# Kernel optimization log

Measured on AMD Instinct MI355X. Metric: run time of the kernel, lower is better.

The kernel has to match this reference:

```python
import jax, jax.numpy as jnp
import numpy as np

GAMMA = 0.5      # temperature from __init__
SOS_ID = 2       # constant <sos> token id
EPS = 1e-10


def setup_inputs() -> dict:
    key = jax.random.key(0)
    ks = jax.random.split(key, 12)
    B, T, E, DY, DZ, V = 64, 32, 100, 200, 500, 32000
    H = DY + DZ
    s = lambda k, shape, sc=1.0: (jax.random.normal(k, shape, jnp.float32) * sc)
    return {
        "z": s(ks[0], (B, DZ), 0.1),
        "labels": jax.random.uniform(ks[1], (B,), jnp.float32),
        "W_fc": s(ks[2], (DY, 1), 0.1),
        "b_fc": s(ks[3], (DY,), 0.1),
        "embed_weight": s(ks[4], (V, E), 0.1),
        "W_ih": s(ks[5], (3 * H, E), 0.05),
        "W_hh": s(ks[6], (3 * H, H), 0.05),
        "b_ih": s(ks[7], (3 * H,), 0.05),
        "b_hh": s(ks[8], (3 * H,), 0.05),
        "W_out": s(ks[9], (V, H), 0.05),
        "b_out": s(ks[10], (V,), 0.05),
        "gumbel_u": jax.random.uniform(ks[11], (T - 1, B, V), jnp.float32),
        "src": jax.random.randint(jax.random.fold_in(key, 99), (T, B), 0, V),
        "src_len": T,
    }


def _gru_step(h, x, W_ih, W_hh, b_ih, b_hh):
    # PyTorch GRU cell: gates ordered (r, z, n)
    gi = x @ W_ih.T + b_ih          # [B, 3H]
    gh = h @ W_hh.T + b_hh          # [B, 3H]
    i_r, i_z, i_n = jnp.split(gi, 3, axis=-1)
    h_r, h_z, h_n = jnp.split(gh, 3, axis=-1)
    r = jax.nn.sigmoid(i_r + h_r)
    zt = jax.nn.sigmoid(i_z + h_z)
    n = jnp.tanh(i_n + r * h_n)
    return (1.0 - zt) * n + zt * h


def reference(z, labels, W_fc, b_fc, embed_weight, W_ih, W_hh, b_ih, b_hh,
              W_out, b_out, gumbel_u, src, src_len):
    B, H = z.shape[0], W_hh.shape[1]
    V = W_out.shape[0]
    # h0 = cat(fc(1 - labels), z)
    h0 = jnp.concatenate([(1.0 - labels)[:, None] @ W_fc.T + b_fc, z], axis=-1)  # [B, H]
    x0 = jnp.broadcast_to(embed_weight[SOS_ID], (B, embed_weight.shape[1]))      # [B, E]

    def step(carry, u):
        h, x = carry
        h = _gru_step(h, x, W_ih, W_hh, b_ih, b_hh)      # [B, H]
        pred = h @ W_out.T + b_out                        # [B, V]
        g = -jnp.log(-jnp.log(u + EPS) + EPS)             # gumbel noise
        y = jax.nn.softmax(pred + g, axis=-1)             # gumbel_softmax, tau=1
        x_next = (y / GAMMA) @ embed_weight               # soft embedding [B, E]
        return (h, x_next), (h, pred)

    (_, _), (outs, preds) = jax.lax.scan(step, (h0, x0), gumbel_u)  # [T-1,B,H], [T-1,B,V]

    dt = z.dtype
    outputs = jnp.concatenate(
        [h0[None], jnp.zeros((1, B, H), dt), outs], axis=0)         # [T+1, B, H]
    predictions = jnp.concatenate(
        [jnp.zeros((1, B, V), dt), preds], axis=0)                  # [T, B, V]
    return outputs, predictions
```

## Files before the change

kernel.cpp:

```cpp
#include <hip/hip_runtime.h>

#define B 64
#define TS 31
#define E 100
#define DY 200
#define DZ 500
#define V 32000
#define H 700
#define HP 704
#define H3 2100
#define XH 800
#define SOS 2
#define OUT_PRED_OFF (33*B*H)
#define NPB 500
#define VCH 125
#define NVCH 256
#define SOFF 15.0f

typedef unsigned short u16;
typedef __attribute__((ext_vector_type(8))) short short8;
typedef __attribute__((ext_vector_type(4))) float f32x4;

__device__ __forceinline__ float sigm(float x) { return 1.f / (1.f + __expf(-x)); }
__device__ __forceinline__ u16 f2b(float f) {
  union { float f; unsigned int u; } c; c.f = f;
  unsigned int u = c.u;
  u16 h = (u16)(u >> 16);
  unsigned int rem = u & 0xFFFFu;
  h += (u16)((rem > 0x8000u) || (rem == 0x8000u && (h & 1)));
  return h;
}

__global__ __launch_bounds__(256) void k_zero(float* __restrict__ out, long n) {
  long i0 = (long)blockIdx.x * 256 + threadIdx.x;
  long st = (long)gridDim.x * 256;
  for (long i = i0; i < n; i += st) out[i] = 0.f;
}

__global__ __launch_bounds__(256) void k0_init(
    const float* __restrict__ z, const float* __restrict__ labels,
    const float* __restrict__ W_fc, const float* __restrict__ b_fc,
    const float* __restrict__ embed, const float* __restrict__ W_ih,
    const float* __restrict__ W_hh, const float* __restrict__ W_out,
    float* __restrict__ out, float* __restrict__ hA, float* __restrict__ WT,
    u16* __restrict__ W2, u16* __restrict__ h_bf,
    float* __restrict__ xacc, float* __restrict__ Zp, float* __restrict__ gh)
{
  long i0 = (long)blockIdx.x * 256 + threadIdx.x;
  long st = (long)gridDim.x * 256;
  for (long i = i0; i < (long)NPB * B; i += st) Zp[i] = 2.f / (float)NPB;
  for (long i = i0; i < (long)B * H3; i += st) gh[i] = 0.f;
  for (long i = i0; i < (long)B * V; i += st) out[OUT_PRED_OFF + i] = 0.f;
  for (long i = i0; i < (long)B * H; i += st) out[B * H + i] = 0.f;
  for (long i = i0; i < (long)B * H; i += st) {
    int b = (int)(i / H), j = (int)(i % H);
    float v = (j < DY) ? (1.f - labels[b]) * W_fc[j] + b_fc[j]
                       : z[b * DZ + (j - DY)];
    hA[i] = v;
    out[i] = v;
  }
  for (long i = i0; i < (long)B * E; i += st) {
    int e = (int)(i % E);
    xacc[i] = embed[SOS * E + e];
  }
  for (long i = i0; i < (long)B * HP; i += st) h_bf[i] = 0;
  for (long i = i0; i < (long)XH * H3; i += st) {
    int k = (int)(i / H3), g = (int)(i % H3);
    WT[i] = (k < E) ? W_ih[(long)g * E + k] : W_hh[(long)g * H + (k - E)];
  }
  for (long i = i0; i < (long)V * HP; i += st) {
    long s8 = i >> 3; int j = (int)(i & 7);
    int lane = (int)(s8 & 63);
    long tmp = s8 >> 6;
    int kk = (int)(tmp % 22);
    long cgrp = tmp / 22;
    int col = (int)(cgrp * 16 + (lane & 15));
    int k = kk * 32 + ((lane >> 4) << 3) + j;
    W2[i] = (k < H) ? f2b(W_out[(size_t)col * H + k]) : (u16)0;
  }
}

__global__ __launch_bounds__(256) void k1a(
    const float* __restrict__ xacc, const float* __restrict__ Zp,
    const float* __restrict__ hin, const float* __restrict__ WT,
    const float* __restrict__ b_ih,
    float* __restrict__ gig, float* __restrict__ gh)
{
  int nt = blockIdx.x, c = blockIdx.y;
  int n = nt * 32 + (threadIdx.x & 31);
  int bq = threadIdx.x >> 5;
  __shared__ float xs[64][100];
  __shared__ float invZ[64];
  if (c == 0) {
    if (threadIdx.x < 64) {
      float s = 0.f;
      for (int u = 0; u < NPB; ++u) s += Zp[(size_t)u * 64 + threadIdx.x];
      invZ[threadIdx.x] = 2.f / s;
    }
    __syncthreads();
  }
  for (int i = threadIdx.x; i < 6400; i += 256) {
    int b = i / 100, kk = i % 100;
    xs[b][kk] = (c == 0) ? xacc[i] * invZ[b] : hin[b * H + (c - 1) * 100 + kk];
  }
  __syncthreads();
  if (n >= H3) return;
  float acc[8];
  #pragma unroll
  for (int bb = 0; bb < 8; ++bb) acc[bb] = 0.f;
  for (int kk = 0; kk < 100; ++kk) {
    float w = WT[(size_t)(c * 100 + kk) * H3 + n];
    #pragma unroll
    for (int bb = 0; bb < 8; ++bb) acc[bb] += xs[bq * 8 + bb][kk] * w;
  }
  if (c == 0) {
    float bi = b_ih[n];
    #pragma unroll
    for (int bb = 0; bb < 8; ++bb) gig[(size_t)(bq * 8 + bb) * H3 + n] = acc[bb] + bi;
  } else {
    #pragma unroll
    for (int bb = 0; bb < 8; ++bb)
      atomicAdd(&gh[(size_t)(bq * 8 + bb) * H3 + n], acc[bb]);
  }
}

__global__ __launch_bounds__(256) void k1br(
    const float* __restrict__ gig, float* __restrict__ gh,
    const float* __restrict__ b_hh, const float* __restrict__ hin,
    float* __restrict__ hout, float* __restrict__ out_h, u16* __restrict__ h_bf,
    float* __restrict__ xacc)
{
  int i = blockIdx.x * 256 + threadIdx.x;
  if (i >= B * H) return;
  if (i < B * E) xacc[i] = 0.f;
  int b = i / H, j = i % H;
  size_t g0 = (size_t)b * H3 + j;
  float ir = gig[g0], iz = gig[g0 + H], in_ = gig[g0 + 2 * H];
  float hr = gh[g0] + b_hh[j];
  float hz = gh[g0 + H] + b_hh[H + j];
  float hn = gh[g0 + 2 * H] + b_hh[2 * H + j];
  gh[g0] = 0.f; gh[g0 + H] = 0.f; gh[g0 + 2 * H] = 0.f;
  float hprev = hin[b * H + j];
  float r  = sigm(ir + hr);
  float zt = sigm(iz + hz);
  float nn = tanhf(in_ + r * hn);
  float hv = (1.f - zt) * nn + zt * hprev;
  hout[b * H + j] = hv;
  out_h[i] = hv;
  h_bf[b * HP + j] = f2b(hv);
}

__global__ __launch_bounds__(256) void k2(
    const u16* __restrict__ h_bf, const u16* __restrict__ W2,
    const float* __restrict__ b_out, const float* __restrict__ gu,
    float* __restrict__ pred, float* __restrict__ w_f, float* __restrict__ Zp)
{
  __shared__ float lzp[64][4];
  const int u = blockIdx.x, tid = threadIdx.x;
  const int wave = tid >> 6, lane = tid & 63, l15 = lane & 15;
  const int col = u * 64 + wave * 16 + l15;
  f32x4 acc[4];
  #pragma unroll
  for (int q = 0; q < 4; ++q) acc[q] = f32x4{0.f, 0.f, 0.f, 0.f};
  const short8* wv2 = (const short8*)W2 + ((size_t)(u * 4 + wave) * 22) * 64 + lane;
  const u16* hp = h_bf + ((lane >> 4) << 3);
  for (int kk = 0; kk < 22; ++kk) {
    short8 bv = wv2[(size_t)kk * 64];
    #pragma unroll
    for (int rt = 0; rt < 4; ++rt) {
      short8 a = *reinterpret_cast<const short8*>(hp + (size_t)(rt * 16 + l15) * HP + kk * 32);
      acc[rt] = __builtin_amdgcn_mfma_f32_16x16x32_bf16(a, bv, acc[rt], 0, 0, 0);
    }
  }
  float bo = b_out[col];
  #pragma unroll
  for (int rt = 0; rt < 4; ++rt) {
    #pragma unroll
    for (int r = 0; r < 4; ++r) {
      int brow = rt * 16 + ((lane >> 4) << 2) + r;
      float pv = acc[rt][r] + bo;
      size_t off = (size_t)brow * V + col;
      __builtin_nontemporal_store(pv, &pred[off]);
      float uu = __builtin_nontemporal_load(&gu[off]);
      float g = -__logf(-__logf(uu + 1e-10f) + 1e-10f);
      float w = __expf(pv + g - SOFF);
      w_f[off] = w;
      float vz = w;
      vz += __shfl_xor(vz, 1); vz += __shfl_xor(vz, 2);
      vz += __shfl_xor(vz, 4); vz += __shfl_xor(vz, 8);
      if (l15 == 0) lzp[brow][wave] = vz;
    }
  }
  __syncthreads();
  if (tid < 64)
    Zp[(size_t)u * 64 + tid] = lzp[tid][0] + lzp[tid][1] + lzp[tid][2] + lzp[tid][3];
}

__global__ __launch_bounds__(256) void k3(
    const float* __restrict__ w_f, const float* __restrict__ embed,
    float* __restrict__ xacc)
{
  int c = blockIdx.x;
  int v0 = c * VCH;
  int e = threadIdx.x & 127, bh = threadIdx.x >> 7;
  __shared__ float ys[64][VCH];
  for (int i = threadIdx.x; i < 64 * VCH; i += 256) {
    int b = i / VCH, vv = i % VCH;
    ys[b][vv] = w_f[(size_t)b * V + v0 + vv];
  }
  __syncthreads();
  if (e >= E) return;
  float acc[32];
  #pragma unroll
  for (int bb = 0; bb < 32; ++bb) acc[bb] = 0.f;
  for (int vv = 0; vv < VCH; ++vv) {
    float w = embed[(size_t)(v0 + vv) * E + e];
    #pragma unroll
    for (int bb = 0; bb < 32; ++bb) acc[bb] += ys[bh * 32 + bb][vv] * w;
  }
  #pragma unroll
  for (int bb = 0; bb < 32; ++bb)
    atomicAdd(&xacc[(size_t)(bh * 32 + bb) * E + e], acc[bb]);
}

extern "C" void kernel_launch(void* const* d_in, const int* in_sizes, int n_in,
                              void* d_out, int out_size, void* d_ws, size_t ws_size,
                              hipStream_t stream) {
  (void)ws_size;
  float* out = (float*)d_out;

  static const long lsz[12] = {32000, 64, 200, 200, 3200000, 210000, 1470000,
                               2100, 2100, 22400000, 32000, 63488000};
  static const int dictP[12]    = {0, 1, 2, 3, 4, 5, 6, 7, 8, 9, 10, 11};
  static const int alpha14P[12] = {13, 10, 0, 4, 8, 2, 1, 6, 5, 3, 7, 9};
  static const int alpha12P[12] = {11, 10, 0, 4, 8, 2, 1, 6, 5, 3, 7, 9};
  auto okperm = [&](const int* p) -> bool {
    for (int i = 0; i < 12; ++i) {
      if (p[i] >= n_in) return false;
      if ((long)in_sizes[p[i]] != lsz[i]) return false;
    }
    return true;
  };
  const int* P_ = nullptr;
  if (okperm(dictP)) P_ = dictP;
  else if (okperm(alpha14P)) P_ = alpha14P;
  else if (okperm(alpha12P)) P_ = alpha12P;
  if (!P_) { k_zero<<<2048, 256, 0, stream>>>(out, (long)out_size); return; }

  const float* z      = (const float*)d_in[P_[0]];
  const float* labels = (const float*)d_in[P_[1]];
  const float* W_fc   = (const float*)d_in[P_[2]];
  const float* b_fc   = (const float*)d_in[P_[3]];
  const float* embed  = (const float*)d_in[P_[4]];
  const float* W_ih   = (const float*)d_in[P_[5]];
  const float* W_hh   = (const float*)d_in[P_[6]];
  const float* b_ih   = (const float*)d_in[P_[7]];
  const float* b_hh   = (const float*)d_in[P_[8]];
  const float* W_out  = (const float*)d_in[P_[9]];
  const float* b_out  = (const float*)d_in[P_[10]];
  const float* gu     = (const float*)d_in[P_[11]];

  char* w = (char*)d_ws;
  auto alloc = [&](size_t bytes) { char* p = w; w += (bytes + 255) & ~(size_t)255; return p; };
  float* hA    = (float*)alloc((size_t)B * H * 4);
  float* hB    = (float*)alloc((size_t)B * H * 4);
  float* WT    = (float*)alloc((size_t)XH * H3 * 4);
  float* gig   = (float*)alloc((size_t)B * H3 * 4);
  float* gh    = (float*)alloc((size_t)B * H3 * 4);
  float* w_f   = (float*)alloc((size_t)B * V * 4);
  float* Zp    = (float*)alloc((size_t)NPB * B * 4);
  float* xacc  = (float*)alloc((size_t)B * E * 4);
  u16*  W2     = (u16*)alloc((size_t)V * HP * 2);
  u16*  h_bf   = (u16*)alloc((size_t)B * HP * 2);

  k0_init<<<2048, 256, 0, stream>>>(z, labels, W_fc, b_fc, embed, W_ih, W_hh, W_out,
                                    out, hA, WT, W2, h_bf, xacc, Zp, gh);

  for (int t = 0; t < TS; ++t) {
    float* hin  = (t & 1) ? hB : hA;
    float* hout = (t & 1) ? hA : hB;
    float* pred = out + OUT_PRED_OFF + (size_t)(1 + t) * B * V;
    k1a<<<dim3(66, 8), 256, 0, stream>>>(xacc, Zp, hin, WT, b_ih, gig, gh);
    k1br<<<(B * H + 255) / 256, 256, 0, stream>>>(gig, gh, b_hh, hin, hout,
                                                  out + (size_t)(2 + t) * B * H, h_bf,
                                                  xacc);
    k2<<<NPB, 256, 0, stream>>>(h_bf, W2, b_out, gu + (size_t)t * B * V,
                                pred, w_f, Zp);
    if (t < TS - 1)
      k3<<<NVCH, 256, 0, stream>>>(w_f, embed, xacc);
  }
}
```

Measured before the change: 3.656 ms.

## Halve k2 block size to 1000 blocks and move softmax-denominator reduction into k3

The vocab-projection kernel now runs 1000 blocks of two waves each instead of 500 blocks of four, so the 32000-column GEMM spreads across more workgroups on the CUs. The per-batch partition-sum reduction, which used to be a serial 500-element loop in k1a's first block, now runs in the otherwise idle threads of k3. Those threads write four partial sums per batch row, and k1a just adds them. This takes a serial reduction off the critical path at the cost of more partial sums and extra work in k3's spare lanes.

New measurement: 5.249 ms. 43.6% more time.

```diff
diff --git a/kernel.cpp b/kernel.cpp
--- a/kernel.cpp
+++ b/kernel.cpp
@@ -12,7 +12,7 @@
 #define XH 800
 #define SOS 2
 #define OUT_PRED_OFF (33*B*H)
-#define NPB 500
+#define NPB2 1000
 #define VCH 125
 #define NVCH 256
 #define SOFF 15.0f
@@ -44,11 +44,11 @@
     const float* __restrict__ W_hh, const float* __restrict__ W_out,
     float* __restrict__ out, float* __restrict__ hA, float* __restrict__ WT,
     u16* __restrict__ W2, u16* __restrict__ h_bf,
-    float* __restrict__ xacc, float* __restrict__ Zp, float* __restrict__ gh)
+    float* __restrict__ xacc, float* __restrict__ ZpH, float* __restrict__ gh)
 {
   long i0 = (long)blockIdx.x * 256 + threadIdx.x;
   long st = (long)gridDim.x * 256;
-  for (long i = i0; i < (long)NPB * B; i += st) Zp[i] = 2.f / (float)NPB;
+  for (long i = i0; i < 4 * B; i += st) ZpH[i] = 0.5f;
   for (long i = i0; i < (long)B * H3; i += st) gh[i] = 0.f;
   for (long i = i0; i < (long)B * V; i += st) out[OUT_PRED_OFF + i] = 0.f;
   for (long i = i0; i < (long)B * H; i += st) out[B * H + i] = 0.f;
@@ -81,7 +81,7 @@
 }
 
 __global__ __launch_bounds__(256) void k1a(
-    const float* __restrict__ xacc, const float* __restrict__ Zp,
+    const float* __restrict__ xacc, const float* __restrict__ ZpH,
     const float* __restrict__ hin, const float* __restrict__ WT,
     const float* __restrict__ b_ih,
     float* __restrict__ gig, float* __restrict__ gh)
@@ -93,9 +93,8 @@
   __shared__ float invZ[64];
   if (c == 0) {
     if (threadIdx.x < 64) {
-      float s = 0.f;
-      for (int u = 0; u < NPB; ++u) s += Zp[(size_t)u * 64 + threadIdx.x];
-      invZ[threadIdx.x] = 2.f / s;
+      const float* zp = ZpH + threadIdx.x * 4;
+      invZ[threadIdx.x] = 2.f / (zp[0] + zp[1] + zp[2] + zp[3]);
     }
     __syncthreads();
   }
@@ -150,19 +149,20 @@
   h_bf[b * HP + j] = f2b(hv);
 }
 
-__global__ __launch_bounds__(256) void k2(
+__global__ __launch_bounds__(128) void k2(
     const u16* __restrict__ h_bf, const u16* __restrict__ W2,
     const float* __restrict__ b_out, const float* __restrict__ gu,
     float* __restrict__ pred, float* __restrict__ w_f, float* __restrict__ Zp)
 {
-  __shared__ float lzp[64][4];
+  __shared__ float lzp[64][2];
   const int u = blockIdx.x, tid = threadIdx.x;
   const int wave = tid >> 6, lane = tid & 63, l15 = lane & 15;
-  const int col = u * 64 + wave * 16 + l15;
+  const int cgrp = u * 2 + wave;
+  const int col = cgrp * 16 + l15;
   f32x4 acc[4];
   #pragma unroll
   for (int q = 0; q < 4; ++q) acc[q] = f32x4{0.f, 0.f, 0.f, 0.f};
-  const short8* wv2 = (const short8*)W2 + ((size_t)(u * 4 + wave) * 22) * 64 + lane;
+  const short8* wv2 = (const short8*)W2 + ((size_t)cgrp * 22) * 64 + lane;
   const u16* hp = h_bf + ((lane >> 4) << 3);
   for (int kk = 0; kk < 22; ++kk) {
     short8 bv = wv2[(size_t)kk * 64];
@@ -193,12 +193,13 @@
   }
   __syncthreads();
   if (tid < 64)
-    Zp[(size_t)u * 64 + tid] = lzp[tid][0] + lzp[tid][1] + lzp[tid][2] + lzp[tid][3];
+    Zp[(size_t)u * 64 + tid] = lzp[tid][0] + lzp[tid][1];
 }
 
 __global__ __launch_bounds__(256) void k3(
     const float* __restrict__ w_f, const float* __restrict__ embed,
-    float* __restrict__ xacc)
+    float* __restrict__ xacc, const float* __restrict__ Zp,
+    float* __restrict__ ZpH)
 {
   int c = blockIdx.x;
   int v0 = c * VCH;
@@ -209,7 +210,16 @@
     ys[b][vv] = w_f[(size_t)b * V + v0 + vv];
   }
   __syncthreads();
-  if (e >= E) return;
+  if (e >= E) {
+    if (e < 102 && c < 64) {
+      int id2 = (e - 100) * 2 + bh;
+      float s = 0.f;
+      for (int u = id2 * 250; u < id2 * 250 + 250; ++u)
+        s += Zp[(size_t)u * 64 + c];
+      ZpH[c * 4 + id2] = s;
+    }
+    return;
+  }
   float acc[32];
   #pragma unroll
   for (int bb = 0; bb < 32; ++bb) acc[bb] = 0.f;
@@ -268,25 +278,26 @@
   float* gig   = (float*)alloc((size_t)B * H3 * 4);
   float* gh    = (float*)alloc((size_t)B * H3 * 4);
   float* w_f   = (float*)alloc((size_t)B * V * 4);
-  float* Zp    = (float*)alloc((size_t)NPB * B * 4);
+  float* Zp    = (float*)alloc((size_t)NPB2 * B * 4);
+  float* ZpH   = (float*)alloc((size_t)4 * B * 4);
   float* xacc  = (float*)alloc((size_t)B * E * 4);
   u16*  W2     = (u16*)alloc((size_t)V * HP * 2);
   u16*  h_bf   = (u16*)alloc((size_t)B * HP * 2);
 
   k0_init<<<2048, 256, 0, stream>>>(z, labels, W_fc, b_fc, embed, W_ih, W_hh, W_out,
-                                    out, hA, WT, W2, h_bf, xacc, Zp, gh);
+                                    out, hA, WT, W2, h_bf, xacc, ZpH, gh);
 
   for (int t = 0; t < TS; ++t) {
     float* hin  = (t & 1) ? hB : hA;
     float* hout = (t & 1) ? hA : hB;
     float* pred = out + OUT_PRED_OFF + (size_t)(1 + t) * B * V;
-    k1a<<<dim3(66, 8), 256, 0, stream>>>(xacc, Zp, hin, WT, b_ih, gig, gh);
+    k1a<<<dim3(66, 8), 256, 0, stream>>>(xacc, ZpH, hin, WT, b_ih, gig, gh);
     k1br<<<(B * H + 255) / 256, 256, 0, stream>>>(gig, gh, b_hh, hin, hout,
                                                   out + (size_t)(2 + t) * B * H, h_bf,
                                                   xacc);
-    k2<<<NPB, 256, 0, stream>>>(h_bf, W2, b_out, gu + (size_t)t * B * V,
-                                pred, w_f, Zp);
+    k2<<<NPB2, 128, 0, stream>>>(h_bf, W2, b_out, gu + (size_t)t * B * V,
+                                 pred, w_f, Zp);
     if (t < TS - 1)
-      k3<<<NVCH, 256, 0, stream>>>(w_f, embed, xacc);
-  }
-}
+      k3<<<NVCH, 256, 0, stream>>>(w_f, embed, xacc, Zp, ZpH);
+  }
+}
```
